# Performance work log

Measured on AMD Instinct MI355X. Metric: run time of the kernel, lower is better.

The kernel has to match this reference:

```python
import jax, jax.numpy as jnp
import numpy as np

NUM_EMBEDDINGS = 8192
EMBEDDING_DIM = 512
COMMITMENT_COST = 0.25
EMA_DECAY = 0.99
EPS = 1e-5


def setup_inputs() -> dict:
    key = jax.random.key(0)
    k1, k2, k3, k4 = jax.random.split(key, 4)
    B = 32768
    z = jax.random.normal(k1, (B, EMBEDDING_DIM), dtype=jnp.float32)
    weight = jax.random.normal(k2, (NUM_EMBEDDINGS, EMBEDDING_DIM), dtype=jnp.float32)
    ema_cluster_size = jax.random.uniform(k3, (NUM_EMBEDDINGS,), dtype=jnp.float32)
    ema_dw = jax.random.normal(k4, (NUM_EMBEDDINGS, EMBEDDING_DIM), dtype=jnp.float32)
    return {"z": z, "weight": weight, "ema_cluster_size": ema_cluster_size, "ema_dw": ema_dw}


def reference(z, weight, ema_cluster_size, ema_dw):
    K = weight.shape[0]
    # Squared-L2 distances: (B, K) = |z|^2 + |e|^2 - 2 z e^T
    distances = (
        jnp.sum(z * z, axis=1, keepdims=True)
        + jnp.sum(weight * weight, axis=1)
        - 2.0 * (z @ weight.T)
    )
    indices = jnp.argmin(distances, axis=1)          # (B,)
    quantized_raw = weight[indices]                  # (B, D) gather

    # EMA codebook update (training-mode buffers; one-hot scatter-add == segment_sum)
    counts = jax.ops.segment_sum(jnp.ones(z.shape[0], dtype=z.dtype), indices, num_segments=K)
    dw = jax.ops.segment_sum(z, indices, num_segments=K)  # encodings.T @ z
    new_cluster_size = ema_cluster_size * EMA_DECAY + (1.0 - EMA_DECAY) * counts
    new_ema_dw = ema_dw * EMA_DECAY + (1.0 - EMA_DECAY) * dw
    n = jnp.sum(new_cluster_size)
    cluster_size = (new_cluster_size + EPS) / (n + K * EPS) * n
    new_weight = new_ema_dw / cluster_size[:, None]

    commitment_loss = COMMITMENT_COST * jnp.mean((z - jax.lax.stop_gradient(quantized_raw)) ** 2)
    quantized = z + jax.lax.stop_gradient(quantized_raw - z)  # straight-through
    return quantized, indices, commitment_loss, new_weight, new_cluster_size, new_ema_dw
```

## Files before the change

### kernel.cpp

```cpp
#include <hip/hip_runtime.h>

#define B_N 32768
#define D_N 512
#define K_N 8192
#define EMA 0.99f
#define ONE_M_EMA 0.01f
#define EPS_ 1e-5f
#define CCOST 0.25f

#define ZP_OFF 295936ull
#define WP_OFF 67404800ull
#define WS_NEED (WP_OFF + 16777216ull)
#define CNT_OFF    295936ull
#define OFFS_OFF   332800ull
#define CURS_OFF   365568ull
#define ROWL_OFF   398336ull
#define LPART_OFF  529408ull

typedef __attribute__((ext_vector_type(8))) short bf16x8;
typedef __attribute__((ext_vector_type(4))) float f32x4;

__global__ __launch_bounds__(256) void prep_kernel(const float* __restrict__ w,
                                                   const float* __restrict__ ecs,
                                                   float* __restrict__ wsq,
                                                   float* __restrict__ ncs_out) {
  int row  = blockIdx.x * 4 + (threadIdx.x >> 6);
  int lane = threadIdx.x & 63;
  const float* p = w + (size_t)row * D_N + lane * 8;
  float4 a = *(const float4*)p;
  float4 b = *(const float4*)(p + 4);
  float s = a.x*a.x + a.y*a.y + a.z*a.z + a.w*a.w
          + b.x*b.x + b.y*b.y + b.z*b.z + b.w*b.w;
  #pragma unroll
  for (int off = 32; off; off >>= 1) s += __shfl_down(s, off);
  if (lane == 0) wsq[row] = s;

  int gid = blockIdx.x * 256 + threadIdx.x;
  if (gid < K_N) ncs_out[gid] = EMA * ecs[gid];
}

__global__ __launch_bounds__(256) void prep_nedw(const float4* __restrict__ edw,
                                                 float4* __restrict__ nedw) {
  int i = blockIdx.x * 256 + threadIdx.x;
  float4 v = edw[i];
  v.x *= EMA; v.y *= EMA; v.z *= EMA; v.w *= EMA;
  nedw[i] = v;
}

__global__ __launch_bounds__(256) void split_z(const float* __restrict__ x,
                                               ushort* __restrict__ xp) {
  int g   = blockIdx.x * 256 + threadIdx.x;
  int row = g >> 6, c = g & 63;
  const float* src = x + (size_t)row * 512 + c * 8;
  float v[8];
  *(float4*)&v[0] = *(const float4*)&src[0];
  *(float4*)&v[4] = *(const float4*)&src[4];
  uint hw[4], lw[4];
  #pragma unroll
  for (int i = 0; i < 4; i++) {
    uint b0 = __float_as_uint(v[2*i]);
    uint b1 = __float_as_uint(v[2*i+1]);
    float r0 = v[2*i]   - __uint_as_float(b0 & 0xFFFF0000u);
    float r1 = v[2*i+1] - __uint_as_float(b1 & 0xFFFF0000u);
    hw[i] = (b0 >> 16) | (b1 & 0xFFFF0000u);
    lw[i] = (__float_as_uint(r0) >> 16) | (__float_as_uint(r1) & 0xFFFF0000u);
  }
  int si  = c >> 2;
  int p   = (c & 3) ^ ((row >> 1) & 3);
  size_t sstr = (size_t)B_N * 32;
  size_t base = (size_t)row * 32 + (size_t)p * 8;
  *(uint4*)&xp[(size_t)si * sstr + base]        = (uint4){hw[0], hw[1], hw[2], hw[3]};
  *(uint4*)&xp[(size_t)(16 + si) * sstr + base] = (uint4){lw[0], lw[1], lw[2], lw[3]};
}

__global__ __launch_bounds__(256) void split_w(const float* __restrict__ x,
                                               ushort* __restrict__ xp,
                                               float* __restrict__ wsq) {
  int g   = blockIdx.x * 256 + threadIdx.x;
  int row = g >> 6, c = g & 63;
  const float* src = x + (size_t)row * 512 + c * 8;
  float v[8];
  *(float4*)&v[0] = *(const float4*)&src[0];
  *(float4*)&v[4] = *(const float4*)&src[4];
  uint hw[4], lw[4]; float w2 = 0.f;
  #pragma unroll
  for (int i = 0; i < 4; i++) {
    uint b0 = __float_as_uint(v[2*i]);
    uint b1 = __float_as_uint(v[2*i+1]);
    float r0 = v[2*i]   - __uint_as_float(b0 & 0xFFFF0000u);
    float r1 = v[2*i+1] - __uint_as_float(b1 & 0xFFFF0000u);
    hw[i] = (b0 >> 16) | (b1 & 0xFFFF0000u);
    lw[i] = (__float_as_uint(r0) >> 16) | (__float_as_uint(r1) & 0xFFFF0000u);
    w2 += v[2*i]*v[2*i] + v[2*i+1]*v[2*i+1];
  }
  int si  = c >> 2;
  int p   = (c & 3) ^ ((row >> 1) & 3);
  size_t sstr = (size_t)K_N * 32;
  size_t base = (size_t)row * 32 + (size_t)p * 8;
  *(uint4*)&xp[(size_t)si * sstr + base]        = (uint4){hw[0], hw[1], hw[2], hw[3]};
  *(uint4*)&xp[(size_t)(16 + si) * sstr + base] = (uint4){lw[0], lw[1], lw[2], lw[3]};
  #pragma unroll
  for (int off = 32; off; off >>= 1) w2 += __shfl_down(w2, off);
  if (c == 0) wsq[row] = w2;
}

constexpr int COLT2 = 8;

#define GLDS(SRC, DST) __builtin_amdgcn_global_load_lds((const unsigned int*)(SRC), (unsigned int*)(DST), 16, 0, 0)

#define PHASE(AC, BC, AL, BL, G)                                               \
  {                                                                            \
    const int g_ = (G);                                                        \
    if (g_ + 1 <= 383) {                                                       \
      const char* Ab_ = (const char*)As[(g_ + 1) & 3] + aoff;                  \
      const char* Bb_ = (const char*)Bs[(g_ + 1) & 3] + boff;                  \
      _Pragma("unroll")                                                        \
      for (int i_ = 0; i_ < 8; i_++) AL[i_] = *(const bf16x8*)(Ab_ + i_ * 1024);\
      _Pragma("unroll")                                                        \
      for (int j_ = 0; j_ < 4; j_++) BL[j_] = *(const bf16x8*)(Bb_ + j_ * 1024);\
    }                                                                          \
    if (g_ + 4 <= 383) {                                                       \
      const int slotF_ = sf & 3;                                               \
      const int zsl_ = (sf < 32) ? (sf & 15) : (sf - 16);      \
      const int wsl_ = (sf < 32) ? sf : (sf - 32);             \
      GLDS(zA + (size_t)zsl_ * 2097152,        (char*)As[slotF_] + t * 16);    \
      GLDS(zA + (size_t)zsl_ * 2097152 + 8192, (char*)As[slotF_] + 8192 + t * 16);\
      const size_t wOfs_ = (size_t)wsl_ * 524288 + (size_t)ctf * 16384;        \
      GLDS(wB + wOfs_,        (char*)Bs[slotF_] + t * 16);                     \
      GLDS(wB + wOfs_ + 8192, (char*)Bs[slotF_] + 8192 + t * 16);              \
      sf++; if (sf == 48) { sf = 0; ctf++; }                                   \
    }                                                                          \
    __builtin_amdgcn_s_setprio(1);                                             \
    _Pragma("unroll")                                                          \
    for (int i_ = 0; i_ < 8; i_++)                                             \
      _Pragma("unroll")                                                        \
      for (int j_ = 0; j_ < 4; j_++)                                           \
        acc[i_][j_] = __builtin_amdgcn_mfma_f32_16x16x32_bf16(AC[i_], BC[j_],  \
                                                        acc[i_][j_], 0, 0, 0); \
    __builtin_amdgcn_s_setprio(0);                                             \
    asm volatile("s_waitcnt lgkmcnt(0)" ::: "memory");                         \
    if (g_ <= 379)      { asm volatile("s_waitcnt vmcnt(8)" ::: "memory"); }   \
    else if (g_ == 380) { asm volatile("s_waitcnt vmcnt(4)" ::: "memory"); }   \
    else if (g_ == 381) { asm volatile("s_waitcnt vmcnt(0)" ::: "memory"); }   \
    __builtin_amdgcn_s_barrier();                                              \
    __builtin_amdgcn_sched_barrier(0);                                         \
  }

__global__ __launch_bounds__(512, 2) void score3p(
    const ushort* __restrict__ zp, const ushort* __restrict__ wp,
    const float* __restrict__ wsq, unsigned long long* __restrict__ packed) {
  __shared__ ushort As[4][8192];
  __shared__ ushort Bs[4][8192];
  __shared__ float wsqs[2048];
  __shared__ unsigned long long best2[256][4];

  const int t = threadIdx.x, lane = t & 63, wid = t >> 6;
  const int wm = wid >> 2, wn = wid & 3;
  const int l15 = lane & 15, lg = (lane >> 4) & 3;
  const int row0 = blockIdx.x * 256;
  const int cg0  = blockIdx.y * 2048;

  const char* zA = (const char*)zp + ((size_t)(row0 + (t >> 2)) * 64 + (size_t)(t & 3) * 16);
  const char* wB = (const char*)wp + ((size_t)(cg0  + (t >> 2)) * 64 + (size_t)(t & 3) * 16);

  const int swz  = (l15 >> 1) & 3;
  const int aoff = (wm * 128 + l15) * 64 + ((lg ^ swz) * 16);
  const int boff = (wn * 64  + l15) * 64 + ((lg ^ swz) * 16);

  { float4 v = *(const float4*)&wsq[cg0 + t * 4]; *(float4*)&wsqs[t * 4] = v; }
  if (t < 256) { best2[t][0] = ~0ull; best2[t][1] = ~0ull; best2[t][2] = ~0ull; best2[t][3] = ~0ull; }
  __syncthreads();

  #pragma unroll
  for (int s0 = 0; s0 < 4; s0++) {
    GLDS(zA + (size_t)s0 * 2097152,        (char*)As[s0] + t * 16);
    GLDS(zA + (size_t)s0 * 2097152 + 8192, (char*)As[s0] + 8192 + t * 16);
    GLDS(wB + (size_t)s0 * 524288,         (char*)Bs[s0] + t * 16);
    GLDS(wB + (size_t)s0 * 524288 + 8192,  (char*)Bs[s0] + 8192 + t * 16);
  }
  asm volatile("s_waitcnt vmcnt(8)" ::: "memory");
  __builtin_amdgcn_s_barrier();
  __builtin_amdgcn_sched_barrier(0);

  bf16x8 aE[8], bE[4], aO[8], bO[4];
  #pragma unroll
  for (int i = 0; i < 8; i++) aE[i] = *(const bf16x8*)((const char*)As[0] + aoff + i * 1024);
  #pragma unroll
  for (int j = 0; j < 4; j++) bE[j] = *(const bf16x8*)((const char*)Bs[0] + boff + j * 1024);
  asm volatile("s_waitcnt lgkmcnt(0)" ::: "memory");
  __builtin_amdgcn_s_barrier();
  __builtin_amdgcn_sched_barrier(0);

  int sf = 4, ctf = 0;

  for (int ct = 0; ct < COLT2; ct++) {
    f32x4 acc[8][4];
    #pragma unroll
    for (int i = 0; i < 8; i++)
      #pragma unroll
      for (int j = 0; j < 4; j++) acc[i][j] = (f32x4){0.f, 0.f, 0.f, 0.f};

    for (int s = 0; s < 48; s += 2) {
      const int g = ct * 48 + s;
      PHASE(aE, bE, aO, bO, g)
      PHASE(aO, bO, aE, bE, g + 1)
    }

    float rv[32]; int rx[32];
    #pragma unroll
    for (int i = 0; i < 8; i++)
      #pragma unroll
      for (int r = 0; r < 4; r++) {
        float bvv = 3.4e38f; int bii = 0;
        #pragma unroll
        for (int j = 0; j < 4; j++) {
          float wq = wsqs[ct * 256 + wn * 64 + j * 16 + l15];
          float dist = wq - 2.0f * acc[i][j][r];
          int c = cg0 + ct * 256 + wn * 64 + j * 16 + l15;
          if (dist < bvv) { bvv = dist; bii = c; }
        }
        rv[i * 4 + r] = bvv; rx[i * 4 + r] = bii;
      }
    #pragma unroll
    for (int e = 0; e < 32; e++) {
      float v = rv[e]; int ix = rx[e];
      #pragma unroll
      for (int m = 1; m < 16; m <<= 1) {
        float ov = __shfl_xor(v, m, 64);
        int   oi = __shfl_xor(ix, m, 64);
        if (ov < v || (ov == v && oi < ix)) { v = ov; ix = oi; }
      }
      rv[e] = v; rx[e] = ix;
    }
    #pragma unroll
    for (int half = 0; half < 2; half++) {
      const int e0 = l15 + half * 16;
      float bvv = 0.f; int bii = 0;
      #pragma unroll
      for (int e = 0; e < 32; e++) {
        bool p = (e == e0);
        bvv = p ? rv[e] : bvv; bii = p ? rx[e] : bii;
      }
      unsigned u = __float_as_uint(bvv);
      u = (u & 0x80000000u) ? ~u : (u | 0x80000000u);
      unsigned long long key = ((unsigned long long)u << 32) | (unsigned)bii;
      const int rowl = wm * 128 + (e0 >> 2) * 16 + lg * 4 + (e0 & 3);
      unsigned long long cur = best2[rowl][wn];
      if (key < cur) best2[rowl][wn] = key;
    }
  }

  __syncthreads();
  if (t < 256) {
    unsigned long long k0 = best2[t][0], k1 = best2[t][1];
    unsigned long long k2 = best2[t][2], k3 = best2[t][3];
    unsigned long long m0 = k0 < k1 ? k0 : k1;
    unsigned long long m1 = k2 < k3 ? k2 : k3;
    atomicMin(&packed[row0 + t], m0 < m1 ? m0 : m1);
  }
}

constexpr int LDP = 40;
constexpr int KSPLIT = 8, COLT = K_N / KSPLIT / 128;
__device__ __forceinline__ void stage16(const float* __restrict__ g,
                                        ushort* __restrict__ h,
                                        ushort* __restrict__ l) {
  float v[16];
  *(float4*)&v[0]  = *(const float4*)&g[0];
  *(float4*)&v[4]  = *(const float4*)&g[4];
  *(float4*)&v[8]  = *(const float4*)&g[8];
  *(float4*)&v[12] = *(const float4*)&g[12];
  uint hw[8], lw[8];
  #pragma unroll
  for (int i = 0; i < 8; i++) {
    uint b0 = __float_as_uint(v[2*i]);
    uint b1 = __float_as_uint(v[2*i+1]);
    float r0 = v[2*i]   - __uint_as_float(b0 & 0xFFFF0000u);
    float r1 = v[2*i+1] - __uint_as_float(b1 & 0xFFFF0000u);
    hw[i] = (b0 >> 16) | (b1 & 0xFFFF0000u);
    lw[i] = (__float_as_uint(r0) >> 16) | (__float_as_uint(r1) & 0xFFFF0000u);
  }
  ((uint4*)h)[0] = *(uint4*)&hw[0];
  ((uint4*)h)[1] = *(uint4*)&hw[4];
  ((uint4*)l)[0] = *(uint4*)&lw[0];
  ((uint4*)l)[1] = *(uint4*)&lw[4];
}

__global__ __launch_bounds__(256, 2) void score_argmin_mfma(
    const float* __restrict__ z, const float* __restrict__ w,
    const float* __restrict__ wsq, unsigned long long* __restrict__ packed) {
  __shared__ ushort Ah[128][LDP];
  __shared__ ushort Al[128][LDP];
  __shared__ ushort Bh[128][LDP];
  __shared__ ushort Bl[128][LDP];
  const int t = threadIdx.x, lane = t & 63, wid = t >> 6;
  const int wm = wid >> 1, wn = wid & 1;
  const int l15 = lane & 15, lg = lane >> 4;
  const int row0 = blockIdx.x * 128;
  const int ks0  = blockIdx.y * (K_N / KSPLIT);
  const int srow = t >> 1, skq = (t & 1) * 16;
  float rmin[16]; int ridx[16];
  #pragma unroll
  for (int e = 0; e < 16; e++) { rmin[e] = 3.4e38f; ridx[e] = 0; }
  for (int ct = 0; ct < COLT; ct++) {
    const int c0 = ks0 + ct * 128;
    f32x4 acc[4][4];
    #pragma unroll
    for (int i = 0; i < 4; i++)
      #pragma unroll
      for (int j = 0; j < 4; j++) acc[i][j] = (f32x4){0.f, 0.f, 0.f, 0.f};
    for (int k0 = 0; k0 < D_N; k0 += 32) {
      __syncthreads();
      stage16(&z[(size_t)(row0 + srow) * D_N + k0 + skq], &Ah[srow][skq], &Al[srow][skq]);
      stage16(&w[(size_t)(c0   + srow) * D_N + k0 + skq], &Bh[srow][skq], &Bl[srow][skq]);
      __syncthreads();
      bf16x8 ah[4], al[4], bh[4], bl[4];
      #pragma unroll
      for (int i = 0; i < 4; i++) {
        ah[i] = *(const bf16x8*)&Ah[wm*64 + i*16 + l15][lg*8];
        al[i] = *(const bf16x8*)&Al[wm*64 + i*16 + l15][lg*8];
        bh[i] = *(const bf16x8*)&Bh[wn*64 + i*16 + l15][lg*8];
        bl[i] = *(const bf16x8*)&Bl[wn*64 + i*16 + l15][lg*8];
      }
      #pragma unroll
      for (int i = 0; i < 4; i++)
        #pragma unroll
        for (int j = 0; j < 4; j++) {
          acc[i][j] = __builtin_amdgcn_mfma_f32_16x16x32_bf16(ah[i], bh[j], acc[i][j], 0, 0, 0);
          acc[i][j] = __builtin_amdgcn_mfma_f32_16x16x32_bf16(ah[i], bl[j], acc[i][j], 0, 0, 0);
          acc[i][j] = __builtin_amdgcn_mfma_f32_16x16x32_bf16(al[i], bh[j], acc[i][j], 0, 0, 0);
        }
    }
    float wq[4];
    #pragma unroll
    for (int j = 0; j < 4; j++) wq[j] = wsq[c0 + wn*64 + j*16 + l15];
    #pragma unroll
    for (int i = 0; i < 4; i++)
      #pragma unroll
      for (int r = 0; r < 4; r++) {
        const int e = i * 4 + r;
        #pragma unroll
        for (int j = 0; j < 4; j++) {
          float dist = wq[j] - 2.0f * acc[i][j][r];
          if (dist < rmin[e]) { rmin[e] = dist; ridx[e] = c0 + wn*64 + j*16 + l15; }
        }
      }
  }
  #pragma unroll
  for (int e = 0; e < 16; e++) {
    float v = rmin[e]; int ix = ridx[e];
    #pragma unroll
    for (int m = 1; m < 16; m <<= 1) {
      float ov = __shfl_xor(v, m, 64);
      int   oi = __shfl_xor(ix, m, 64);
      if (ov < v || (ov == v && oi < ix)) { v = ov; ix = oi; }
    }
    rmin[e] = v; ridx[e] = ix;
  }
  const int s = l15;
  float bv = 0.f; int bi = 0;
  #pragma unroll
  for (int e = 0; e < 16; e++) {
    bool p = (e == s);
    bv = p ? rmin[e] : bv;
    bi = p ? ridx[e] : bi;
  }
  unsigned u = __float_as_uint(bv);
  u = (u & 0x80000000u) ? ~u : (u | 0x80000000u);
  unsigned long long key = ((unsigned long long)u << 32) | (unsigned)bi;
  atomicMin(&packed[row0 + wm*64 + (s >> 2)*16 + lg*4 + (s & 3)], key);
}

__global__ __launch_bounds__(256) void count_kernel(
    const unsigned long long* __restrict__ packed, int* __restrict__ cnt,
    float* __restrict__ idxout) {
  int row = blockIdx.x * 256 + threadIdx.x;
  int idx = (int)(packed[row] & 0xFFFFFFFFull);
  idxout[row] = (float)idx;
  atomicAdd(&cnt[idx], 1);
}

__global__ __launch_bounds__(256) void scan_kernel(const int* __restrict__ cnt,
                                                   int* __restrict__ offs,
                                                   int* __restrict__ cursor) {
  int t = threadIdx.x;
  int base = t * 32;
  int local[32];
  int s = 0;
  #pragma unroll
  for (int i = 0; i < 32; i++) { local[i] = s; s += cnt[base + i]; }
  __shared__ int ps[257];
  ps[t + 1] = s;
  if (t == 0) ps[0] = 0;
  __syncthreads();
  if (t == 0) { for (int i = 1; i <= 256; i++) ps[i] += ps[i - 1]; }
  __syncthreads();
  int e = ps[t];
  #pragma unroll
  for (int i = 0; i < 32; i++) {
    int o = e + local[i];
    offs[base + i] = o; cursor[base + i] = o;
  }
  if (t == 255) offs[8192] = ps[256];
}

__global__ __launch_bounds__(256) void scatter_ids(
    const unsigned long long* __restrict__ packed, int* __restrict__ cursor,
    int* __restrict__ rowlist) {
  int row = blockIdx.x * 256 + threadIdx.x;
  int idx = (int)(packed[row] & 0xFFFFFFFFull);
  int pos = atomicAdd(&cursor[idx], 1);
  rowlist[pos] = row;
}

__global__ __launch_bounds__(256) void seg_accum(
    const float* __restrict__ z, const float* __restrict__ edw,
    const float* __restrict__ ecs, const int* __restrict__ offs,
    const int* __restrict__ rowlist, float* __restrict__ nedw_out,
    float* __restrict__ ncs_out) {
  int k = blockIdx.x, t = threadIdx.x;
  int s0 = offs[k], s1 = offs[k + 1];
  float ax = 0.f, ay = 0.f;
  for (int r = s0; r < s1; r++) {
    int row = rowlist[r];
    float2 zv = *(const float2*)&z[(size_t)row * D_N + t * 2];
    ax += zv.x; ay += zv.y;
  }
  float2 ev = *(const float2*)&edw[(size_t)k * D_N + t * 2];
  float2 o;
  o.x = EMA * ev.x + ONE_M_EMA * ax;
  o.y = EMA * ev.y + ONE_M_EMA * ay;
  *(float2*)&nedw_out[(size_t)k * D_N + t * 2] = o;
  if (t == 0) ncs_out[k] = EMA * ecs[k] + ONE_M_EMA * (float)(s1 - s0);
}

__global__ __launch_bounds__(256) void quant_loss(
    const float* __restrict__ z, const float* __restrict__ w,
    const unsigned long long* __restrict__ packed,
    float* __restrict__ qout, float* __restrict__ lpart) {
  int row = blockIdx.x, t = threadIdx.x;
  int idx = (int)(packed[row] & 0xFFFFFFFFull);
  float2 zv = *(const float2*)&z[(size_t)row * D_N + t * 2];
  float2 wv = *(const float2*)&w[(size_t)idx * D_N + t * 2];
  float2 q;
  q.x = zv.x + (wv.x - zv.x);
  q.y = zv.y + (wv.y - zv.y);
  *(float2*)&qout[(size_t)row * D_N + t * 2] = q;
  float dx = zv.x - wv.x, dy = zv.y - wv.y;
  float s = dx * dx + dy * dy;
  #pragma unroll
  for (int off = 32; off; off >>= 1) s += __shfl_down(s, off);
  __shared__ float part[4];
  if ((t & 63) == 0) part[t >> 6] = s;
  __syncthreads();
  if (t == 0) lpart[row] = part[0] + part[1] + part[2] + part[3];
}

__global__ __launch_bounds__(256) void reduce2(const float* __restrict__ ncs_out,
                                               const float* __restrict__ lpart,
                                               float* __restrict__ nsum,
                                               float* __restrict__ loss_sum) {
  int t = threadIdx.x;
  float s1 = 0.f, s2 = 0.f;
  for (int i = t; i < K_N; i += 256) s1 += ncs_out[i];
  for (int i = t; i < B_N; i += 256) s2 += lpart[i];
  #pragma unroll
  for (int off = 32; off; off >>= 1) {
    s1 += __shfl_down(s1, off);
    s2 += __shfl_down(s2, off);
  }
  __shared__ float p1[4], p2[4];
  if ((t & 63) == 0) { p1[t >> 6] = s1; p2[t >> 6] = s2; }
  __syncthreads();
  if (t == 0) {
    nsum[0]     = p1[0] + p1[1] + p1[2] + p1[3];
    loss_sum[0] = p2[0] + p2[1] + p2[2] + p2[3];
  }
}

__global__ __launch_bounds__(256) void gather_scatter(
    const float* __restrict__ z, const float* __restrict__ w,
    const unsigned long long* __restrict__ packed,
    float* __restrict__ qout, float* __restrict__ idxout,
    float* __restrict__ ncs_out, float* __restrict__ nedw_out,
    float* __restrict__ loss_sum) {
  int row = blockIdx.x;
  int t   = threadIdx.x;
  int idx = (int)(packed[row] & 0xFFFFFFFFull);
  float2 zv = *(const float2*)&z[(size_t)row * D_N + t * 2];
  float2 wv = *(const float2*)&w[(size_t)idx * D_N + t * 2];
  float2 q;
  q.x = zv.x + (wv.x - zv.x);
  q.y = zv.y + (wv.y - zv.y);
  *(float2*)&qout[(size_t)row * D_N + t * 2] = q;
  float dx = zv.x - wv.x, dy = zv.y - wv.y;
  float s = dx*dx + dy*dy;
  #pragma unroll
  for (int off = 32; off; off >>= 1) s += __shfl_down(s, off);
  __shared__ float part[4];
  if ((t & 63) == 0) part[t >> 6] = s;
  __syncthreads();
  if (t == 0) {
    atomicAdd(loss_sum, part[0] + part[1] + part[2] + part[3]);
    atomicAdd(&ncs_out[idx], ONE_M_EMA);
    idxout[row] = (float)idx;
  }
  atomicAdd(&nedw_out[(size_t)idx * D_N + t*2],     ONE_M_EMA * zv.x);
  atomicAdd(&nedw_out[(size_t)idx * D_N + t*2 + 1], ONE_M_EMA * zv.y);
}

__global__ __launch_bounds__(256) void reduce_n(const float* __restrict__ ncs_out,
                                                float* __restrict__ nsum) {
  int t = threadIdx.x;
  float s = 0.f;
  for (int i = t; i < K_N; i += 256) s += ncs_out[i];
  #pragma unroll
  for (int off = 32; off; off >>= 1) s += __shfl_down(s, off);
  __shared__ float part[4];
  if ((t & 63) == 0) part[t >> 6] = s;
  __syncthreads();
  if (t == 0) nsum[0] = part[0] + part[1] + part[2] + part[3];
}

__global__ __launch_bounds__(256) void finalize(
    const float* __restrict__ ncs_out, const float* __restrict__ nedw_out,
    float* __restrict__ nw_out, const float* __restrict__ nsum,
    const float* __restrict__ loss_sum, float* __restrict__ loss_out) {
  size_t i = (size_t)blockIdx.x * 256 + threadIdx.x;
  float n = nsum[0];
  int k = (int)(i >> 9);
  float nv = ncs_out[k];
  float cs = (nv + EPS_) / (n + K_N * EPS_) * n;
  nw_out[i] = nedw_out[i] / cs;
  if (i == 0) loss_out[0] = CCOST * loss_sum[0] / (float)((size_t)B_N * D_N);
}

extern "C" void kernel_launch(void* const* d_in, const int* in_sizes, int n_in,
                              void* d_out, int out_size, void* d_ws, size_t ws_size,
                              hipStream_t stream) {
  const float* z   = (const float*)d_in[0];
  const float* w   = (const float*)d_in[1];
  const float* ecs = (const float*)d_in[2];
  const float* edw = (const float*)d_in[3];

  float* out      = (float*)d_out;
  float* qout     = out;
  float* idxout   = out + (size_t)B_N * D_N;
  float* loss_out = idxout + B_N;
  float* nw_out   = loss_out + 1;
  float* ncs_out  = nw_out + (size_t)K_N * D_N;
  float* nedw_out = ncs_out + K_N;

  unsigned long long* packed = (unsigned long long*)d_ws;
  float* wsq      = (float*)((char*)d_ws + 262144);
  float* loss_sum = (float*)((char*)d_ws + 294912);
  float* nsum     = loss_sum + 1;

  hipMemsetAsync(d_ws, 0xFF, 262144, stream);
  hipMemsetAsync((void*)loss_sum, 0, 8, stream);

  if (ws_size >= WS_NEED) {
    ushort* zp  = (ushort*)((char*)d_ws + ZP_OFF);
    ushort* wp  = (ushort*)((char*)d_ws + WP_OFF);
    int* cnt    = (int*)((char*)d_ws + CNT_OFF);
    int* offs   = (int*)((char*)d_ws + OFFS_OFF);
    int* cursor = (int*)((char*)d_ws + CURS_OFF);
    int* rowl   = (int*)((char*)d_ws + ROWL_OFF);
    float* lpart= (float*)((char*)d_ws + LPART_OFF);

    split_z<<<8192, 256, 0, stream>>>(z, zp);
    split_w<<<2048, 256, 0, stream>>>(w, wp, wsq);
    score3p<<<dim3(128, 4), 512, 0, stream>>>(zp, wp, wsq, packed);
    hipMemsetAsync((void*)cnt, 0, K_N * sizeof(int), stream);
    count_kernel<<<B_N / 256, 256, 0, stream>>>(packed, cnt, idxout);
    scan_kernel<<<1, 256, 0, stream>>>(cnt, offs, cursor);
    scatter_ids<<<B_N / 256, 256, 0, stream>>>(packed, cursor, rowl);
    seg_accum<<<K_N, 256, 0, stream>>>(z, edw, ecs, offs, rowl, nedw_out, ncs_out);
    quant_loss<<<B_N, 256, 0, stream>>>(z, w, packed, qout, lpart);
    reduce2<<<1, 256, 0, stream>>>(ncs_out, lpart, nsum, loss_sum);
  } else {
    prep_kernel<<<2048, 256, 0, stream>>>(w, ecs, wsq, ncs_out);
    prep_nedw<<<4096, 256, 0, stream>>>((const float4*)edw, (float4*)nedw_out);
    score_argmin_mfma<<<dim3(B_N / 128, KSPLIT), 256, 0, stream>>>(z, w, wsq, packed);
    gather_scatter<<<B_N, 256, 0, stream>>>(z, w, packed, qout, idxout,
                                            ncs_out, nedw_out, loss_sum);
    reduce_n<<<1, 256, 0, stream>>>(ncs_out, nsum);
  }

  finalize<<<K_N * D_N / 256, 256, 0, stream>>>(ncs_out, nedw_out, nw_out,
                                                nsum, loss_sum, loss_out);
}
```

Measured before the change: 1.023 ms.

## Process two K-steps per barrier in the MFMA score pipeline

Restructures the score kernel's main loop so each barrier-delimited phase stages two LDS slots with global_load_lds, runs two MFMA blocks, and interleaves the LDS fragment loads for the next two steps between them. This halves the number of workgroup barriers and waitcnt points per column tile and gives the LDS reads more MFMA work to hide behind. In exchange, each phase now waits for all outstanding global loads (vmcnt(0)) instead of keeping a partial queue in flight. That shortens the effective prefetch distance and may expose global load latency.

```diff
diff --git a/kernel.cpp b/kernel.cpp
--- a/kernel.cpp
+++ b/kernel.cpp
@@ -108,45 +108,59 @@
 
 #define GLDS(SRC, DST) __builtin_amdgcn_global_load_lds((const unsigned int*)(SRC), (unsigned int*)(DST), 16, 0, 0)
 
-#define PHASE(AC, BC, AL, BL, G)                                               \
+#define STAGE1(S, SL)                                                          \
   {                                                                            \
-    const int g_ = (G);                                                        \
-    if (g_ + 1 <= 383) {                                                       \
-      const char* Ab_ = (const char*)As[(g_ + 1) & 3] + aoff;                  \
-      const char* Bb_ = (const char*)Bs[(g_ + 1) & 3] + boff;                  \
-      _Pragma("unroll")                                                        \
-      for (int i_ = 0; i_ < 8; i_++) AL[i_] = *(const bf16x8*)(Ab_ + i_ * 1024);\
-      _Pragma("unroll")                                                        \
-      for (int j_ = 0; j_ < 4; j_++) BL[j_] = *(const bf16x8*)(Bb_ + j_ * 1024);\
-    }                                                                          \
-    if (g_ + 4 <= 383) {                                                       \
-      const int slotF_ = sf & 3;                                               \
-      const int zsl_ = (sf < 32) ? (sf & 15) : (sf - 16);      \
-      const int wsl_ = (sf < 32) ? sf : (sf - 32);             \
-      GLDS(zA + (size_t)zsl_ * 2097152,        (char*)As[slotF_] + t * 16);    \
-      GLDS(zA + (size_t)zsl_ * 2097152 + 8192, (char*)As[slotF_] + 8192 + t * 16);\
-      const size_t wOfs_ = (size_t)wsl_ * 524288 + (size_t)ctf * 16384;        \
-      GLDS(wB + wOfs_,        (char*)Bs[slotF_] + t * 16);                     \
-      GLDS(wB + wOfs_ + 8192, (char*)Bs[slotF_] + 8192 + t * 16);              \
-      sf++; if (sf == 48) { sf = 0; ctf++; }                                   \
-    }                                                                          \
+    const int s__ = (S);                                                       \
+    const int zsl_ = (s__ < 32) ? (s__ & 15) : (s__ - 16);     \
+    const int wsl_ = (s__ < 32) ? s__ : (s__ - 32);            \
+    GLDS(zA + (size_t)zsl_ * 2097152,        (char*)As[SL] + t * 16);          \
+    GLDS(zA + (size_t)zsl_ * 2097152 + 8192, (char*)As[SL] + 8192 + t * 16);   \
+    const size_t wOfs_ = (size_t)wsl_ * 524288 + (size_t)ctf * 16384;          \
+    GLDS(wB + wOfs_,        (char*)Bs[SL] + t * 16);                           \
+    GLDS(wB + wOfs_ + 8192, (char*)Bs[SL] + 8192 + t * 16);                    \
+  }
+
+#define LOADFRAG(AX, BX, G)                                                    \
+  {                                                                            \
+    const char* Ab_ = (const char*)As[(G) & 3] + aoff;                         \
+    const char* Bb_ = (const char*)Bs[(G) & 3] + boff;                         \
+    _Pragma("unroll")                                                          \
+    for (int i_ = 0; i_ < 8; i_++) AX[i_] = *(const bf16x8*)(Ab_ + i_ * 1024); \
+    _Pragma("unroll")                                                          \
+    for (int j_ = 0; j_ < 4; j_++) BX[j_] = *(const bf16x8*)(Bb_ + j_ * 1024); \
+  }
+
+#define MFMABLK(AX, BX)                                                        \
+  {                                                                            \
     __builtin_amdgcn_s_setprio(1);                                             \
     _Pragma("unroll")                                                          \
     for (int i_ = 0; i_ < 8; i_++)                                             \
       _Pragma("unroll")                                                        \
       for (int j_ = 0; j_ < 4; j_++)                                           \
-        acc[i_][j_] = __builtin_amdgcn_mfma_f32_16x16x32_bf16(AC[i_], BC[j_],  \
+        acc[i_][j_] = __builtin_amdgcn_mfma_f32_16x16x32_bf16(AX[i_], BX[j_],  \
                                                         acc[i_][j_], 0, 0, 0); \
     __builtin_amdgcn_s_setprio(0);                                             \
+  }
+
+#define PHASE2(G2)                                                             \
+  {                                                                            \
+    const int g2_ = (G2);                                                      \
+    if (g2_ + 4 <= 383) {                         \
+      STAGE1(sf,     sf & 3)                                                   \
+      STAGE1(sf + 1, (sf + 1) & 3)                                             \
+      sf += 2; if (sf == 48) { sf = 0; ctf++; }                                \
+    }                                                                          \
+    MFMABLK(aE, bE)                                              \
+    if (g2_ + 2 <= 383) LOADFRAG(aE, bE, g2_ + 2)    \
+    MFMABLK(aO, bO)                                            \
+    if (g2_ + 3 <= 383) LOADFRAG(aO, bO, g2_ + 3)                              \
     asm volatile("s_waitcnt lgkmcnt(0)" ::: "memory");                         \
-    if (g_ <= 379)      { asm volatile("s_waitcnt vmcnt(8)" ::: "memory"); }   \
-    else if (g_ == 380) { asm volatile("s_waitcnt vmcnt(4)" ::: "memory"); }   \
-    else if (g_ == 381) { asm volatile("s_waitcnt vmcnt(0)" ::: "memory"); }   \
+    asm volatile("s_waitcnt vmcnt(0)" ::: "memory");                           \
     __builtin_amdgcn_s_barrier();                                              \
     __builtin_amdgcn_sched_barrier(0);                                         \
   }
 
-__global__ __launch_bounds__(512, 2) void score3p(
+__global__ __launch_bounds__(512, 2) void score3r(
     const ushort* __restrict__ zp, const ushort* __restrict__ wp,
     const float* __restrict__ wsq, unsigned long long* __restrict__ packed) {
   __shared__ ushort As[4][8192];
@@ -171,6 +185,8 @@
   if (t < 256) { best2[t][0] = ~0ull; best2[t][1] = ~0ull; best2[t][2] = ~0ull; best2[t][3] = ~0ull; }
   __syncthreads();
 
+  int sf = 4, ctf = 0;
+
   #pragma unroll
   for (int s0 = 0; s0 < 4; s0++) {
     GLDS(zA + (size_t)s0 * 2097152,        (char*)As[s0] + t * 16);
@@ -178,21 +194,17 @@
     GLDS(wB + (size_t)s0 * 524288,         (char*)Bs[s0] + t * 16);
     GLDS(wB + (size_t)s0 * 524288 + 8192,  (char*)Bs[s0] + 8192 + t * 16);
   }
-  asm volatile("s_waitcnt vmcnt(8)" ::: "memory");
+  asm volatile("s_waitcnt vmcnt(0)" ::: "memory");
   __builtin_amdgcn_s_barrier();
   __builtin_amdgcn_sched_barrier(0);
 
   bf16x8 aE[8], bE[4], aO[8], bO[4];
-  #pragma unroll
-  for (int i = 0; i < 8; i++) aE[i] = *(const bf16x8*)((const char*)As[0] + aoff + i * 1024);
-  #pragma unroll
-  for (int j = 0; j < 4; j++) bE[j] = *(const bf16x8*)((const char*)Bs[0] + boff + j * 1024);
+  LOADFRAG(aE, bE, 0)
+  LOADFRAG(aO, bO, 1)
   asm volatile("s_waitcnt lgkmcnt(0)" ::: "memory");
   __builtin_amdgcn_s_barrier();
   __builtin_amdgcn_sched_barrier(0);
 
-  int sf = 4, ctf = 0;
-
   for (int ct = 0; ct < COLT2; ct++) {
     f32x4 acc[8][4];
     #pragma unroll
@@ -200,10 +212,8 @@
       #pragma unroll
       for (int j = 0; j < 4; j++) acc[i][j] = (f32x4){0.f, 0.f, 0.f, 0.f};
 
-    for (int s = 0; s < 48; s += 2) {
-      const int g = ct * 48 + s;
-      PHASE(aE, bE, aO, bO, g)
-      PHASE(aO, bO, aE, bE, g + 1)
+    for (int p = 0; p < 24; p++) {
+      PHASE2(ct * 48 + 2 * p)
     }
 
     float rv[32]; int rx[32];
@@ -238,8 +248,8 @@
       float bvv = 0.f; int bii = 0;
       #pragma unroll
       for (int e = 0; e < 32; e++) {
-        bool p = (e == e0);
-        bvv = p ? rv[e] : bvv; bii = p ? rx[e] : bii;
+        bool p2 = (e == e0);
+        bvv = p2 ? rv[e] : bvv; bii = p2 ? rx[e] : bii;
       }
       unsigned u = __float_as_uint(bvv);
       u = (u & 0x80000000u) ? ~u : (u | 0x80000000u);
@@ -570,7 +580,7 @@
 
     split_z<<<8192, 256, 0, stream>>>(z, zp);
     split_w<<<2048, 256, 0, stream>>>(w, wp, wsq);
-    score3p<<<dim3(128, 4), 512, 0, stream>>>(zp, wp, wsq, packed);
+    score3r<<<dim3(128, 4), 512, 0, stream>>>(zp, wp, wsq, packed);
     hipMemsetAsync((void*)cnt, 0, K_N * sizeof(int), stream);
     count_kernel<<<B_N / 256, 256, 0, stream>>>(packed, cnt, idxout);
     scan_kernel<<<1, 256, 0, stream>>>(cnt, offs, cursor);
```

After: 1.019 ms (median of 2 runs). About the same (-0.4%).
